# Optimization experiments

Measured on AMD Instinct MI355X. Metric: run time of the kernel, lower is better.

The kernel has to match this reference:

```python
import jax, jax.numpy as jnp
import numpy as np

# dims: batch, history P, horizon Q, hidden D, nodes N, cells C=H*W, Z channels
B_, P_, Q_, D_, N_, C_, H_, W_, CZ = 16, 12, 12, 64, 2000, 1024, 32, 32, 2
K_DIFF = 3  # max diffusion step of DCGRUCell -> K+1 Chebyshev terms


def _mlp2(x, w1, b1, w2, b2):
    return jax.nn.relu(x @ w1 + b1) @ w2 + b2


def _st_embedding(SE, TE, sw1, sb1, sw2, sb2, tw1, tb1, tw2, tb2):
    # GMAN-style spatio-temporal embedding: SE (M,D), TE (B,P,2) ints
    se = _mlp2(SE, sw1, sb1, sw2, sb2)                                  # (M, D)
    te = jnp.concatenate([jax.nn.one_hot(TE[..., 0], 7, dtype=SE.dtype),
                          jax.nn.one_hot(TE[..., 1], 288, dtype=SE.dtype)], axis=-1)
    te = _mlp2(te, tw1, tb1, tw2, tb2)                                  # (B, P, D)
    return se[None, None] + te[:, :, None, :]                           # (B, P, M, D)


def _scaled_laplacian(adj):
    # DCRNN 'laplacian' filter: L_tilde = 2 L / lambda_max - I, lambda_max ~= 2
    A = jnp.maximum(adj, adj.T)
    d = A.sum(axis=1)
    dinv = jnp.where(d > 0, jax.lax.rsqrt(d), 0.0)
    eye = jnp.eye(A.shape[0], dtype=A.dtype)
    L = eye - (dinv[:, None] * A) * dinv[None, :]
    return L - eye


def _gconv(x, L, K):
    # Chebyshev diffusion features: x (B,N,F) -> (B,N,F*(K+1))
    xs = [x, jnp.einsum('nm,bmf->bnf', L, x)]
    for _ in range(2, K + 1):
        xs.append(2.0 * jnp.einsum('nm,bmf->bnf', L, xs[-1]) - xs[-2])
    b, n, f = x.shape
    return jnp.stack(xs, axis=-1).reshape(b, n, f * (K + 1))


def _hard_sigmoid(x):
    return jnp.clip(0.2 * x + 0.5, 0.0, 1.0)


def _conv2d(x, w):
    return jax.lax.conv_general_dilated(x, w, (1, 1), 'SAME',
        dimension_numbers=('NHWC', 'HWIO', 'NHWC'))


def _forward(X, Z, TE, adj_gg, adj_gr, gumbel_noise, se_x, se_z, movement_logits,
             stex_se_w1, stex_se_b1, stex_se_w2, stex_se_b2,
             stex_te_w1, stex_te_b1, stex_te_w2, stex_te_b2,
             stez_se_w1, stez_se_b1, stez_se_w2, stez_se_b2,
             stez_te_w1, stez_te_b1, stez_te_w2, stez_te_b2,
             fcs_z_w1, fcs_z_b1, fcs_z_w2, fcs_z_b2,
             fcs_x_in_w1, fcs_x_in_b1, fcs_x_in_w2, fcs_x_in_b2,
             mov_fc_w, mov_fc_b,
             fcs_x_out_w1, fcs_x_out_b1, fcs_x_out_w2, fcs_x_out_b2,
             convlstm_wx, convlstm_wh,
             dcgru_gate_w, dcgru_gate_b, dcgru_cand_w, dcgru_cand_b):
    B = X.shape[0]
    TEp = TE.astype(jnp.int32)[:, :P_, :]
    # --- cell branch ---
    STEZ = _st_embedding(se_z, TEp, stez_se_w1, stez_se_b1, stez_se_w2, stez_se_b2,
                         stez_te_w1, stez_te_b1, stez_te_w2, stez_te_b2)
    Zf = _mlp2(Z, fcs_z_w1, fcs_z_b1, fcs_z_w2, fcs_z_b2) + STEZ          # (B,P,C,D)
    Zg = Zf.reshape(B, P_, H_, W_, D_)
    def clstm_step(carry, x):
        h, c = carry
        gates = _conv2d(x, convlstm_wx) + _conv2d(h, convlstm_wh)         # (B,H,W,4D)
        i, f, g, o = jnp.split(gates, 4, axis=-1)
        c = _hard_sigmoid(f) * c + _hard_sigmoid(i) * jnp.tanh(g)
        h = _hard_sigmoid(o) * jnp.tanh(c)
        return (h, c), h
    hc0 = (jnp.zeros((B, H_, W_, D_), X.dtype), jnp.zeros((B, H_, W_, D_), X.dtype))
    _, hs = jax.lax.scan(clstm_step, hc0, jnp.swapaxes(Zg, 0, 1))
    Zc = jnp.swapaxes(hs, 0, 1).reshape(B, P_, C_, D_)
    # gumbel-softmax routing over cells (soft, tau=1)
    g = -jnp.log(-jnp.log(gumbel_noise + 1e-20) + 1e-20)
    mZ = jax.nn.softmax(movement_logits + g, axis=-1)                     # (C,C)
    Zc = jnp.einsum('cd,bpdk->bpck', mZ, Zc)
    Zc = jax.nn.relu(Zc @ mov_fc_w + mov_fc_b)
    ZX = jnp.einsum('nc,bpck->bpnk', adj_gr, Zc)                          # (B,P,N,D)
    # --- node branch ---
    STEX = _st_embedding(se_x, TEp, stex_se_w1, stex_se_b1, stex_se_w2, stex_se_b2,
                         stex_te_w1, stex_te_b1, stex_te_w2, stex_te_b2)
    Xf = _mlp2(X[..., None], fcs_x_in_w1, fcs_x_in_b1, fcs_x_in_w2, fcs_x_in_b2) + STEX + ZX
    L = _scaled_laplacian(adj_gg)
    def dcgru_step(h, x):
        xh = jnp.concatenate([x, h], axis=-1)                             # (B,N,2D)
        ru = jax.nn.sigmoid(_gconv(xh, L, K_DIFF) @ dcgru_gate_w + dcgru_gate_b)
        r, u = jnp.split(ru, 2, axis=-1)
        cnd = jnp.tanh(_gconv(jnp.concatenate([x, r * h], axis=-1), L, K_DIFF)
                       @ dcgru_cand_w + dcgru_cand_b)
        return u * h + (1.0 - u) * cnd, None
    h_last, _ = jax.lax.scan(dcgru_step, jnp.zeros((B, N_, D_), X.dtype),
                             jnp.swapaxes(Xf, 0, 1))                      # (B,N,D)
    Y = _mlp2(h_last, fcs_x_out_w1, fcs_x_out_b1, fcs_x_out_w2, fcs_x_out_b2)  # (B,N,Q)
    return jnp.transpose(Y, (0, 2, 1))                                    # (B,Q,N)


def setup_inputs() -> dict:
    key = jax.random.key(0)
    ks = iter(jax.random.split(key, 64))
    def rn(shape, s=0.05):
        return jax.random.normal(next(ks), shape, dtype=jnp.float32) * s
    def ru(shape):
        return jax.random.uniform(next(ks), shape, dtype=jnp.float32)
    z = lambda *s: jnp.zeros(s, jnp.float32)
    NM = K_DIFF + 1
    inp = {
        'X': rn((B_, P_, N_), 1.0),
        'Z': rn((B_, P_, C_, CZ), 1.0),
        'TE': jax.random.randint(next(ks), (B_, P_ + Q_, 2), 0, 7, dtype=jnp.int32),
        'adj_gg': ru((N_, N_)),
        'adj_gr': ru((N_, C_)) * 0.01,
        'gumbel_noise': jnp.clip(ru((C_, C_)), 1e-6, 1.0 - 1e-6),
        'se_x': rn((N_, D_)), 'se_z': rn((C_, D_)),
        'movement_logits': rn((C_, C_)),
        'stex_se_w1': rn((D_, D_)), 'stex_se_b1': z(D_), 'stex_se_w2': rn((D_, D_)), 'stex_se_b2': z(D_),
        'stex_te_w1': rn((295, D_)), 'stex_te_b1': z(D_), 'stex_te_w2': rn((D_, D_)), 'stex_te_b2': z(D_),
        'stez_se_w1': rn((D_, D_)), 'stez_se_b1': z(D_), 'stez_se_w2': rn((D_, D_)), 'stez_se_b2': z(D_),
        'stez_te_w1': rn((295, D_)), 'stez_te_b1': z(D_), 'stez_te_w2': rn((D_, D_)), 'stez_te_b2': z(D_),
        'fcs_z_w1': rn((CZ, D_)), 'fcs_z_b1': z(D_), 'fcs_z_w2': rn((D_, D_)), 'fcs_z_b2': z(D_),
        'fcs_x_in_w1': rn((1, D_)), 'fcs_x_in_b1': z(D_), 'fcs_x_in_w2': rn((D_, D_)), 'fcs_x_in_b2': z(D_),
        'mov_fc_w': rn((D_, D_)), 'mov_fc_b': z(D_),
        'fcs_x_out_w1': rn((D_, D_)), 'fcs_x_out_b1': z(D_), 'fcs_x_out_w2': rn((D_, Q_)), 'fcs_x_out_b2': z(Q_),
        'convlstm_wx': rn((3, 3, D_, 4 * D_)), 'convlstm_wh': rn((3, 3, D_, 4 * D_)),
        'dcgru_gate_w': rn((2 * D_ * NM, 2 * D_)), 'dcgru_gate_b': z(2 * D_),
        'dcgru_cand_w': rn((2 * D_ * NM, D_)), 'dcgru_cand_b': z(D_),
    }
    return inp


def reference(X, Z, TE, adj_gg, adj_gr, gumbel_noise, se_x, se_z, movement_logits,
              stex_se_w1, stex_se_b1, stex_se_w2, stex_se_b2,
              stex_te_w1, stex_te_b1, stex_te_w2, stex_te_b2,
              stez_se_w1, stez_se_b1, stez_se_w2, stez_se_b2,
              stez_te_w1, stez_te_b1, stez_te_w2, stez_te_b2,
              fcs_z_w1, fcs_z_b1, fcs_z_w2, fcs_z_b2,
              fcs_x_in_w1, fcs_x_in_b1, fcs_x_in_w2, fcs_x_in_b2,
              mov_fc_w, mov_fc_b,
              fcs_x_out_w1, fcs_x_out_b1, fcs_x_out_w2, fcs_x_out_b2,
              convlstm_wx, convlstm_wh,
              dcgru_gate_w, dcgru_gate_b, dcgru_cand_w, dcgru_cand_b):
    return _forward(X, Z, TE, adj_gg, adj_gr, gumbel_noise, se_x, se_z, movement_logits,
                    stex_se_w1, stex_se_b1, stex_se_w2, stex_se_b2,
                    stex_te_w1, stex_te_b1, stex_te_w2, stex_te_b2,
                    stez_se_w1, stez_se_b1, stez_se_w2, stez_se_b2,
                    stez_te_w1, stez_te_b1, stez_te_w2, stez_te_b2,
                    fcs_z_w1, fcs_z_b1, fcs_z_w2, fcs_z_b2,
                    fcs_x_in_w1, fcs_x_in_b1, fcs_x_in_w2, fcs_x_in_b2,
                    mov_fc_w, mov_fc_b,
                    fcs_x_out_w1, fcs_x_out_b1, fcs_x_out_w2, fcs_x_out_b2,
                    convlstm_wx, convlstm_wh,
                    dcgru_gate_w, dcgru_gate_b, dcgru_cand_w, dcgru_cand_b)
```

## Files before the change

kernel.cpp:

```cpp
#include <hip/hip_runtime.h>
#include <hip/hip_bf16.h>
#include <math.h>

typedef _Float16 fp16;
typedef _Float16 f16x8 __attribute__((ext_vector_type(8)));
typedef float f32x4 __attribute__((ext_vector_type(4)));

#define BB 16
#define PP 12
#define QQ 12
#define NN 2000
#define CC 1024
#define GP 34
#define GP2 1156

static __device__ __forceinline__ float ldf(float v) { return v; }
static __device__ __forceinline__ float ldf(fp16 v) { return (float)v; }
static __device__ __forceinline__ void stf(float* p, float v) { *p = v; }
static __device__ __forceinline__ void stf(fp16* p, float v) { *p = (fp16)v; }

static __device__ __forceinline__ void gload_lds16(const fp16* g, fp16* l) {
  __builtin_amdgcn_global_load_lds(
      (const __attribute__((address_space(1))) void*)g,
      (__attribute__((address_space(3))) void*)l, 16, 0, 0);
}

__global__ void k_f2h(fp16* __restrict__ dst, const float* __restrict__ src, long long n) {
  long long i = (long long)blockIdx.x * 256 + threadIdx.x;
  if (i < n) dst[i] = (fp16)src[i];
}

__global__ void k_wcatT(fp16* __restrict__ dst, const float* __restrict__ w39,
                        const float* __restrict__ w40) {
  int i = blockIdx.x * 256 + threadIdx.x;
  if (i >= 1152 * 256) return;
  int n = i & 255, kk = i >> 8;
  float v = (kk < 576) ? w39[kk * 256 + n] : w40[(kk - 576) * 256 + n];
  dst[(long long)n * 1152 + kk] = (fp16)v;
}

__global__ void k_gru_repackT(fp16* __restrict__ dst, const float* __restrict__ src, int O) {
  int i = blockIdx.x * 256 + threadIdx.x;
  if (i >= O * 512) return;
  int d = i >> 9;
  int kc = i & 511;
  int t = kc >> 7;
  int c = kc & 127;
  dst[i] = (fp16)src[(c * 4 + t) * O + d];
}

__global__ void k_w2T(fp16* __restrict__ dst, const float* __restrict__ src) {
  int i = blockIdx.x * 256 + threadIdx.x;
  if (i >= 4096) return;
  int d = i >> 6, k = i & 63;
  dst[i] = (fp16)src[k * 64 + d];
}

__global__ void k_dinv(const float* __restrict__ adj, float* __restrict__ dinv) {
  int row = blockIdx.x;
  float s = 0.f;
  for (int j = threadIdx.x; j < NN; j += 256)
    s += fmaxf(adj[(long long)row * NN + j], adj[(long long)j * NN + row]);
  __shared__ float red[256];
  red[threadIdx.x] = s;
  __syncthreads();
  for (int st = 128; st > 0; st >>= 1) {
    if (threadIdx.x < st) red[threadIdx.x] += red[threadIdx.x + st];
    __syncthreads();
  }
  if (threadIdx.x == 0) {
    float d = red[0];
    dinv[row] = d > 0.f ? 1.0f / sqrtf(d) : 0.f;
  }
}

__global__ void k_L(const float* __restrict__ adj, const float* __restrict__ dinv,
                    fp16* __restrict__ Lh) {
  long long i = (long long)blockIdx.x * 256 + threadIdx.x;
  if (i >= (long long)NN * NN) return;
  int r = (int)(i / NN), c = (int)(i % NN);
  float a = fmaxf(adj[(long long)r * NN + c], adj[(long long)c * NN + r]);
  Lh[(long long)r * 2048 + c] = (fp16)(-dinv[r] * a * dinv[c]);
}

__global__ void k_subdiag(fp16* __restrict__ M2) {
  int i = blockIdx.x * 256 + threadIdx.x;
  if (i >= NN) return;
  M2[(long long)i * 2048 + i] = (fp16)((float)M2[(long long)i * 2048 + i] - 1.0f);
}

__global__ void k_gumbel_softmax(const float* __restrict__ ml, const float* __restrict__ gn,
                                 fp16* __restrict__ mZ) {
  int row = blockIdx.x;
  __shared__ float buf[CC];
  __shared__ float red[256];
  int t = threadIdx.x;
  float mx = -1e30f;
  for (int j = t; j < CC; j += 256) {
    float u = gn[(long long)row * CC + j];
    float g = -logf(-logf(u + 1e-20f) + 1e-20f);
    float v = ml[(long long)row * CC + j] + g;
    buf[j] = v;
    mx = fmaxf(mx, v);
  }
  red[t] = mx;
  __syncthreads();
  for (int st = 128; st > 0; st >>= 1) {
    if (t < st) red[t] = fmaxf(red[t], red[t + st]);
// ... 78 lines not shown
  float acc[4][4] = {};
  for (int k0 = 0; k0 < K; k0 += 16) {
#pragma unroll
    for (int j = 0; j < 4; ++j) {
      int e = tid + 256 * j;
      int m = e >> 4, kk = e & 15;
      int gm = row0 + m;
      As[kk][m] = (gm < M) ? ldf(A[(long long)gm * lda + k0 + kk]) : 0.f;
    }
#pragma unroll
    for (int j = 0; j < 4; ++j) {
      int e = tid + 256 * j;
      int kk = e >> 6, n = e & 63;
      int gn = col0 + n;
      Bs[kk][n] = (gn < Ncols) ? ldf(Bm[(long long)(k0 + kk) * ldb + gn]) : 0.f;
    }
    __syncthreads();
#pragma unroll
    for (int kk = 0; kk < 16; ++kk) {
      float a[4], bb[4];
#pragma unroll
      for (int i = 0; i < 4; ++i) a[i] = As[kk][ty * 4 + i];
#pragma unroll
      for (int j = 0; j < 4; ++j) bb[j] = Bs[kk][tx * 4 + j];
#pragma unroll
      for (int i = 0; i < 4; ++i)
#pragma unroll
        for (int j = 0; j < 4; ++j) acc[i][j] = fmaf(a[i], bb[j], acc[i][j]);
    }
    __syncthreads();
  }
#pragma unroll
  for (int i = 0; i < 4; ++i) {
    int r = row0 + ty * 4 + i;
    if (r >= M) continue;
#pragma unroll
    for (int j = 0; j < 4; ++j) {
      int cn = col0 + tx * 4 + j;
      if (cn >= Ncols) continue;
      float v = alpha * acc[i][j];
      if (bias) v += bias[cn];
      if (S) v += beta * ldf(S[(long long)r * ldc + cn]);
      if (act == 1) v = fmaxf(v, 0.f);
      else if (act == 2) v = 1.f / (1.f + expf(-v));
      else if (act == 3) v = tanhf(v);
      stf(&Cm[(long long)r * ldc + cn], v);
    }
  }
}

template <int MT, int MODE>
__global__ __launch_bounds__(256) void mfma7(
    const fp16* __restrict__ A,
    const fp16* __restrict__ U0base, long long uZ, int bHi,
    const fp16* __restrict__ xB, long long xZ,
    const fp16* __restrict__ Xc, long long XcSlab, int Xcld, int Xczmul,
    const fp16* __restrict__ Hc, long long HcSlab, int Hcld, int Hczmul,
    fp16* __restrict__ C, int ldc, long long cBatch,
    const float* __restrict__ bias,
    fp16* __restrict__ rhOut, const fp16* __restrict__ hIn,
    const fp16* __restrict__ uIn, long long uStride,
    int M, int Ncols) {
  __shared__ fp16 As[2][MT * 32];
  __shared__ fp16 Bs[2][64 * 32];
  const int z = blockIdx.z;
  const int n0 = blockIdx.y * 64;
  const fp16* U0z = U0base + (long long)z * uZ;
  const fp16* xBz = xB + (long long)z * xZ;
  C += (long long)z * cBatch;
  if (rhOut) rhOut += (long long)z * uZ;
  if (hIn) hIn += (long long)z * uZ;
  if (uIn) uIn += (long long)z * uStride;
  const int tid = threadIdx.x;
  const int lane = tid & 63, wv = tid >> 6;
  const int wr = wv >> 1, wc = wv & 1;
  const int quad = lane >> 4, ln = lane & 15;
  constexpr int WM = MT / 32;

  const fp16* aSrc[MT / 64];
#pragma unroll
  for (int i = 0; i < MT / 64; ++i) {
    int c = i * 256 + tid;
    int row = c >> 2;
    int lseg = (c & 3) ^ (row & 3);
    aSrc[i] = A + (long long)row * 512 + lseg * 8;
  }
  const int brow = tid >> 2;
  const int blseg = (tid & 3) ^ (brow & 3);
  const long long bnode = n0 + brow;

  f32x4 acc[WM][2];
#pragma unroll
  for (int i = 0; i < WM; ++i)
#pragma unroll
    for (int j = 0; j < 2; ++j) acc[i][j] = (f32x4){0.f, 0.f, 0.f, 0.f};

  auto stage = [&](int t, int buf) {
    const int k0 = t * 32;
#pragma unroll
    for (int i = 0; i < MT / 64; ++i)
      gload_lds16(aSrc[i] + k0, &As[buf][(i * 256 + tid) * 8]);
    if (k0 < 128) {
      int kin = k0 + (tid & 31);
      int ngrp = tid >> 5;
      int n = n0 + ngrp * 8;
      const fp16* src = (kin < 64) ? (xBz + (long long)kin * 2048 + n)
                                   : (U0z + (long long)(kin + bHi) * 2048 + n);
      f16x8 v = *(const f16x8*)src;
      int kk = tid & 31;
#pragma unroll
      for (int j = 0; j < 8; ++j) {
        int rn = ngrp * 8 + j;
        Bs[buf][rn * 32 + ((((kk >> 3) ^ (rn & 3)) << 3) | (kk & 7))] = v[j];
      }
    } else {
      int slab = k0 >> 7;
      int kin = (k0 & 127) + blseg * 8;
      const fp16* src;
      if (kin < 64)
        src = Xc + (long long)(slab - 1) * XcSlab + bnode * Xcld +
              (long long)z * Xczmul + kin;
      else
        src = Hc + (long long)(slab - 1) * HcSlab + bnode * Hcld +
              (long long)z * Hczmul + (kin - 64);
      gload_lds16(src, &Bs[buf][tid * 8]);
    }
  };

  const int sw = (quad ^ (ln & 3)) << 3;
  stage(0, 0);
  for (int t = 0; t < 16; ++t) {
    const int buf = t & 1;
    __syncthreads();
    if (t + 1 < 16) stage(t + 1, buf ^ 1);
    f16x8 af[WM], bf[2];
#pragma unroll
    for (int wm = 0; wm < WM; ++wm) {
      int row = wr * (MT / 2) + wm * 16 + ln;
      af[wm] = *(const f16x8*)&As[buf][row * 32 + sw];
    }
#pragma unroll
    for (int wn = 0; wn < 2; ++wn) {
      int row = wc * 32 + wn * 16 + ln;
      bf[wn] = *(const f16x8*)&Bs[buf][row * 32 + sw];
    }
#pragma unroll
    for (int wm = 0; wm < WM; ++wm)
#pragma unroll
      for (int wn = 0; wn < 2; ++wn)
        acc[wm][wn] =
            __builtin_amdgcn_mfma_f32_16x16x32_f16(af[wm], bf[wn], acc[wm][wn], 0, 0, 0);
  }
#pragma unroll
  for (int wm = 0; wm < WM; ++wm) {
#pragma unroll
    for (int wn = 0; wn < 2; ++wn) {
#pragma unroll
      for (int r = 0; r < 4; ++r) {
        int gm = wr * (MT / 2) + wm * 16 + quad * 4 + r;
        int gn = n0 + wc * 32 + wn * 16 + ln;
        if (gm < M && gn < Ncols) {
          float v = acc[wm][wn][r];
          v += bias[gm];
          if (MODE == 1) {
            v = 1.f / (1.f + expf(-v));
            C[(long long)gm * ldc + gn] = (fp16)v;
            if (gm < 64) {
              float h = (float)hIn[(long long)gm * 2048 + gn];
              rhOut[(long long)gm * 2048 + gn] = (fp16)(v * h);
            }
          } else {
            v = tanhf(v);
            float u = (float)uIn[(long long)(64 + gm) * NN + gn];
            long long ci = (long long)gm * ldc + gn;
            float h = (float)C[ci];
            C[ci] = (fp16)(u * h + (1.f - u) * v);
          }
        }
      }
    }
  }
}

template <int MT, int NT>
__global__ __launch_bounds__(256) void mfma3(
    const fp16* __restrict__ A, int lda, long long zA, int aMsh, long long aMslab,
    const fp16* __restrict__ B, int ldb, long long zB,
    fp16* __restrict__ C, int ldc, long long zC, int cMsh, long long cMslab, int cNsh,
    long long cNslab,
    const fp16* __restrict__ S, long long zS, float beta,
    const float* __restrict__ rowBias, long long zRB,
    const float* __restrict__ s2T, int s2ld,
    int M, int Ncols, int K, float alpha, int act) {
  __shared__ fp16 As[MT][40];
  __shared__ fp16 Bs[NT][40];
  const int z = blockIdx.z;
  const int gm0 = blockIdx.x * MT, n0 = blockIdx.y * NT;
  A += (long long)z * zA;
  B += (long long)z * zB;
  C += (long long)z * zC;
  if (S) S += (long long)z * zS;
  const int tid = threadIdx.x;
  const int lane = tid & 63, wv = tid >> 6;
  const int wr = wv >> 1, wc = wv & 1;
  const int quad = lane >> 4, ln = lane & 15;
  const unsigned aMmask = (1u << aMsh) - 1u;
  const unsigned cMmask = (1u << cMsh) - 1u;
  const unsigned cNmask = (1u << cNsh) - 1u;
  constexpr int WM = MT / 32, WN = NT / 32;
  f32x4 acc[WM][WN];
#pragma unroll
  for (int i = 0; i < WM; ++i)
// ... 23 lines not shown
      int n = c >> 2, seg = c & 3;
      int gn = n0 + n;
      int kk0 = k0 + seg * 8;
      const fp16* src = B + (long long)gn * ldb + kk0;
      if (gn < Ncols && kk0 + 8 <= K) {
        *(f16x8*)&Bs[n][seg * 8] = *(const f16x8*)src;
      } else {
#pragma unroll
        for (int j = 0; j < 8; ++j)
          Bs[n][seg * 8 + j] = (gn < Ncols && kk0 + j < K) ? src[j] : (fp16)0.f;
      }
    }
    __syncthreads();
    f16x8 af[WM], bf[WN];
#pragma unroll
    for (int wm = 0; wm < WM; ++wm)
      af[wm] = *(const f16x8*)&As[wr * (MT / 2) + wm * 16 + ln][quad * 8];
#pragma unroll
    for (int wn = 0; wn < WN; ++wn)
      bf[wn] = *(const f16x8*)&Bs[wc * (NT / 2) + wn * 16 + ln][quad * 8];
#pragma unroll
    for (int wm = 0; wm < WM; ++wm)
#pragma unroll
      for (int wn = 0; wn < WN; ++wn)
        acc[wm][wn] =
            __builtin_amdgcn_mfma_f32_16x16x32_f16(af[wm], bf[wn], acc[wm][wn], 0, 0, 0);
    __syncthreads();
  }
#pragma unroll
  for (int wm = 0; wm < WM; ++wm) {
#pragma unroll
    for (int wn = 0; wn < WN; ++wn) {
#pragma unroll
      for (int r = 0; r < 4; ++r) {
        int gm = gm0 + wr * (MT / 2) + wm * 16 + quad * 4 + r;
        int gn = n0 + wc * (NT / 2) + wn * 16 + ln;
        if (gm < M && gn < Ncols) {
          float v = alpha * acc[wm][wn][r];
          if (rowBias) v += rowBias[(long long)z * zRB + gm];
          if (s2T) v += s2T[(long long)gn * s2ld + gm];
          long long ci = ((long long)((unsigned)gm >> cMsh)) * cMslab +
                         (long long)(gm & cMmask) * ldc +
                         ((long long)((unsigned)gn >> cNsh)) * cNslab + (gn & cNmask);
          if (S) v += beta * (float)S[ci];
          if (act == 1) v = fmaxf(v, 0.f);
          else if (act == 2) v = 1.f / (1.f + expf(-v));
          else if (act == 3) v = tanhf(v);
          C[ci] = (fp16)v;
        }
      }
    }
  }
}

template <int MT, int NT>
__global__ __launch_bounds__(256) void mfma4(
    const fp16* __restrict__ base0, const fp16* __restrict__ base1, int rsh, int ssh,
    long long z0, long long z1, int lda,
    const fp16* __restrict__ B, int ldb, long long zB,
    fp16* __restrict__ C, int ldc, long long zC, int cMsh, long long cMslab, int cNsh,
    long long cNslab,
    const fp16* __restrict__ S, float alpha, float beta, int K) {
  __shared__ fp16 As[2][MT * 32];
  __shared__ fp16 Bs[2][NT * 32];
  const int tid = threadIdx.x;
  const int z = blockIdx.z;
  const int gm0 = blockIdx.x * MT, n0 = blockIdx.y * NT;
  B += (long long)z * zB;
  C += (long long)z * zC;
  if (S) S += (long long)z * zC;
  const unsigned cMmask = (1u << cMsh) - 1u;
  const unsigned cNmask = (1u << cNsh) - 1u;
  const int lane = tid & 63, wv = tid >> 6;
  const int wr = wv >> 1, wc = wv & 1;
  const int quad = lane >> 4, ln = lane & 15;
  constexpr int WM = MT / 32, WN = NT / 32;

  const fp16* aSrc[MT / 64];
  const fp16* bSrc[NT / 64];
#pragma unroll
  for (int i = 0; i < MT / 64; ++i) {
    int c = i * 256 + tid;
    int row = c >> 2;
    int lseg = (c & 3) ^ (row & 3);
    int gm = gm0 + row;
    unsigned b = (unsigned)gm >> rsh;
    unsigned wi = (unsigned)gm & ((1u << rsh) - 1u);
    unsigned sel = wi >> ssh;
    unsigned r = wi & ((1u << ssh) - 1u);
    const fp16* ab = sel ? (base1 + (long long)b * z1) : (base0 + (long long)b * z0);
    aSrc[i] = ab + (long long)r * lda + lseg * 8;
  }
#pragma unroll
  for (int i = 0; i < NT / 64; ++i) {
    int c = i * 256 + tid;
    int row = c >> 2;
    int lseg = (c & 3) ^ (row & 3);
    bSrc[i] = B + (long long)(n0 + row) * ldb + lseg * 8;
  }

  f32x4 acc[WM][WN];
#pragma unroll
  for (int i = 0; i < WM; ++i)
#pragma unroll
    for (int j = 0; j < WN; ++j) acc[i][j] = (f32x4){0.f, 0.f, 0.f, 0.f};

  const int sw = (quad ^ (ln & 3)) << 3;

#pragma unroll
  for (int i = 0; i < MT / 64; ++i) gload_lds16(aSrc[i], &As[0][(i * 256 + tid) * 8]);
#pragma unroll
  for (int i = 0; i < NT / 64; ++i) gload_lds16(bSrc[i], &Bs[0][(i * 256 + tid) * 8]);

  const int nk = K >> 5;
  for (int t = 0; t < nk; ++t) {
    const int buf = t & 1;
    __syncthreads();
    if (t + 1 < nk) {
      const int k1 = (t + 1) * 32;
#pragma unroll
      for (int i = 0; i < MT / 64; ++i)
        gload_lds16(aSrc[i] + k1, &As[buf ^ 1][(i * 256 + tid) * 8]);
#pragma unroll
      for (int i = 0; i < NT / 64; ++i)
        gload_lds16(bSrc[i] + k1, &Bs[buf ^ 1][(i * 256 + tid) * 8]);
    }
    f16x8 af[WM], bf[WN];
#pragma unroll
    for (int wm = 0; wm < WM; ++wm) {
      int row = wr * (MT / 2) + wm * 16 + ln;
      af[wm] = *(const f16x8*)&As[buf][row * 32 + sw];
    }
#pragma unroll
    for (int wn = 0; wn < WN; ++wn) {
      int row = wc * (NT / 2) + wn * 16 + ln;
      bf[wn] = *(const f16x8*)&Bs[buf][row * 32 + sw];
    }
#pragma unroll
    for (int wm = 0; wm < WM; ++wm)
#pragma unroll
      for (int wn = 0; wn < WN; ++wn)
        acc[wm][wn] =
            __builtin_amdgcn_mfma_f32_16x16x32_f16(af[wm], bf[wn], acc[wm][wn], 0, 0, 0);
  }
#pragma unroll
  for (int wm = 0; wm < WM; ++wm)
#pragma unroll
    for (int wn = 0; wn < WN; ++wn)
#pragma unroll
      for (int r = 0; r < 4; ++r) {
        int gm = gm0 + wr * (MT / 2) + wm * 16 + quad * 4 + r;
        int gn = n0 + wc * (NT / 2) + wn * 16 + ln;
        long long ci = ((long long)((unsigned)gm >> cMsh)) * cMslab +
                       (long long)(gm & cMmask) * ldc +
                       ((long long)((unsigned)gn >> cNsh)) * cNslab + (gn & cNmask);
        float v = alpha * acc[wm][wn][r];
        if (S) v += beta * (float)S[ci];
        C[ci] = (fp16)v;
      }
}

template <int MT, int NT>
__global__ __launch_bounds__(256) void mfma6(
    const fp16* __restrict__ A, int lda,
    const fp16* __restrict__ b0, const fp16* __restrict__ b1, int rsh, int ssh,
    long long z0, long long z1, int ldb,
    fp16* __restrict__ C, int ldc, int cMsh, long long cMslab,
    int K) {
  __shared__ fp16 As[2][MT * 32];
  __shared__ fp16 Bs[2][NT * 32];
  const int tid = threadIdx.x;
  const int gm0 = blockIdx.x * MT, n0 = blockIdx.y * NT;
  const unsigned cMmask = (1u << cMsh) - 1u;
  const int lane = tid & 63, wv = tid >> 6;
  const int wr = wv >> 1, wc = wv & 1;
  const int quad = lane >> 4, ln = lane & 15;
  constexpr int WM = MT / 32, WN = NT / 32;

  const fp16* aSrc[MT / 64];
  const fp16* bSrc[NT / 64];
#pragma unroll
  for (int i = 0; i < MT / 64; ++i) {
    int c = i * 256 + tid;
    int row = c >> 2;
    int lseg = (c & 3) ^ (row & 3);
    aSrc[i] = A + (long long)(gm0 + row) * lda + lseg * 8;
  }
#pragma unroll
  for (int i = 0; i < NT / 64; ++i) {
    int c = i * 256 + tid;
    int row = c >> 2;
    int lseg = (c & 3) ^ (row & 3);
    int gn = n0 + row;
    unsigned b = (unsigned)gn >> rsh;
    unsigned wi = (unsigned)gn & ((1u << rsh) - 1u);
    unsigned sel = wi >> ssh;
    unsigned r = wi & ((1u << ssh) - 1u);
    const fp16* bb = sel ? (b1 + (long long)b * z1) : (b0 + (long long)b * z0);
    bSrc[i] = bb + (long long)r * ldb + lseg * 8;
  }

  f32x4 acc[WM][WN];
#pragma unroll
  for (int i = 0; i < WM; ++i)
#pragma unroll
    for (int j = 0; j < WN; ++j) acc[i][j] = (f32x4){0.f, 0.f, 0.f, 0.f};

  const int sw = (quad ^ (ln & 3)) << 3;

#pragma unroll
  for (int i = 0; i < MT / 64; ++i) gload_lds16(aSrc[i], &As[0][(i * 256 + tid) * 8]);
#pragma unroll
  for (int i = 0; i < NT / 64; ++i) gload_lds16(bSrc[i], &Bs[0][(i * 256 + tid) * 8]);

  const int nk = K >> 5;
  for (int t = 0; t < nk; ++t) {
    const int buf = t & 1;
    __syncthreads();
    if (t + 1 < nk) {
      const int k1 = (t + 1) * 32;
#pragma unroll
      for (int i = 0; i < MT / 64; ++i)
        gload_lds16(aSrc[i] + k1, &As[buf ^ 1][(i * 256 + tid) * 8]);
#pragma unroll
      for (int i = 0; i < NT / 64; ++i)
        gload_lds16(bSrc[i] + k1, &Bs[buf ^ 1][(i * 256 + tid) * 8]);
    }
    f16x8 af[WM], bf[WN];
#pragma unroll
    for (int wm = 0; wm < WM; ++wm) {
      int row = wr * (MT / 2) + wm * 16 + ln;
      af[wm] = *(const f16x8*)&As[buf][row * 32 + sw];
    }
#pragma unroll
    for (int wn = 0; wn < WN; ++wn) {
      int row = wc * (NT / 2) + wn * 16 + ln;
      bf[wn] = *(const f16x8*)&Bs[buf][row * 32 + sw];
    }
#pragma unroll
    for (int wm = 0; wm < WM; ++wm)
#pragma unroll
      for (int wn = 0; wn < WN; ++wn)
        acc[wm][wn] =
            __builtin_amdgcn_mfma_f32_16x16x32_f16(af[wm], bf[wn], acc[wm][wn], 0, 0, 0);
  }
#pragma unroll
  for (int wm = 0; wm < WM; ++wm)
#pragma unroll
    for (int wn = 0; wn < WN; ++wn)
#pragma unroll
      for (int r = 0; r < 4; ++r) {
        int gm = gm0 + wr * (MT / 2) + wm * 16 + quad * 4 + r;
        int gn = n0 + wc * (NT / 2) + wn * 16 + ln;
        long long ci = ((long long)((unsigned)gm >> cMsh)) * cMslab +
                       (long long)(gm & cMmask) * ldc + gn;
        C[ci] = (fp16)acc[wm][wn][r];
      }
}

__global__ __launch_bounds__(256) void k_zxtfin(
    const fp16* __restrict__ w2T, const fp16* __restrict__ Tmat,
    fp16* __restrict__ ZXt, const float* __restrict__ teXb, const float* __restrict__ seX) {
  __shared__ fp16 As[64][72];
  __shared__ fp16 Bs[128][72];
  const int z = blockIdx.z;
  const int n0 = blockIdx.y * 128;
  const fp16* Tz = Tmat + (long long)z * 2048 * 64;
  fp16* Cz = ZXt + (long long)z * 64 * 2048;
  const float* tb = teXb + z * 64;
  const int tid = threadIdx.x;
  const int lane = tid & 63, wv = tid >> 6;
  const int wr = wv >> 1, wc = wv & 1;
  const int quad = lane >> 4, ln = lane & 15;
#pragma unroll
  for (int i = 0; i < 2; ++i) {
    int c = tid + 256 * i;
    int row = c >> 3, seg = c & 7;
    *(f16x8*)&As[row][seg * 8] = *(const f16x8*)(w2T + row * 64 + seg * 8);
  }
#pragma unroll
  for (int i = 0; i < 4; ++i) {
    int c = tid + 256 * i;
    int row = c >> 3, seg = c & 7;
    *(f16x8*)&Bs[row][seg * 8] =
        *(const f16x8*)(Tz + (long long)(n0 + row) * 64 + seg * 8);
  }
  __syncthreads();
  f32x4 acc[2][4];
#pragma unroll
  for (int i = 0; i < 2; ++i)
#pragma unroll
    for (int j = 0; j < 4; ++j) acc[i][j] = (f32x4){0.f, 0.f, 0.f, 0.f};
#pragma unroll
  for (int kt = 0; kt < 2; ++kt) {
    f16x8 af[2], bf[4];
#pragma unroll
    for (int wm = 0; wm < 2; ++wm)
      af[wm] = *(const f16x8*)&As[wr * 32 + wm * 16 + ln][kt * 32 + quad * 8];
#pragma unroll
    for (int wn = 0; wn < 4; ++wn)
      bf[wn] = *(const f16x8*)&Bs[wc * 64 + wn * 16 + ln][kt * 32 + quad * 8];
#pragma unroll
    for (int wm = 0; wm < 2; ++wm)
#pragma unroll
      for (int wn = 0; wn < 4; ++wn)
        acc[wm][wn] =
            __builtin_amdgcn_mfma_f32_16x16x32_f16(af[wm], bf[wn], acc[wm][wn], 0, 0, 0);
  }
#pragma unroll
  for (int wm = 0; wm < 2; ++wm)
#pragma unroll
    for (int wn = 0; wn < 4; ++wn)
#pragma unroll
      for (int r = 0; r < 4; ++r) {
        int gm = wr * 32 + wm * 16 + quad * 4 + r;
        int gn = n0 + wc * 64 + wn * 16 + ln;
        long long ci = (long long)gm * 2048 + gn;
        float v = 0.f;
        if (gn < NN)
          v = acc[wm][wn][r] + (float)Cz[ci] + tb[gm] + seX[(long long)gn * 64 + gm];
        Cz[ci] = (fp16)v;
      }
}

__global__ __launch_bounds__(256) void k_conv4(
    const fp16* __restrict__ Zfp, const fp16* __restrict__ hp,
    const fp16* __restrict__ wcatT, fp16* __restrict__ gates, int p) {
  __shared__ fp16 As[2][128 * 32];
  __shared__ fp16 Bs[2][64 * 32];
  const int gm0 = blockIdx.x * 128, n0 = blockIdx.y * 64;
  const int tid = threadIdx.x;
  const int lane = tid & 63, wv = tid >> 6;
  const int wr = wv >> 1, wc = wv & 1;
  const int quad = lane >> 4, ln = lane & 15;

  long long aZ[2], aH[2];
#pragma unroll
  for (int i = 0; i < 2; ++i) {
    int c = tid + 256 * i;
    int row = c >> 2;
    int lseg = (c & 3) ^ (row & 3);
    int m = gm0 + row;
    int b = m >> 10, y = (m >> 5) & 31, x = m & 31;
    int pc = (y + 1) * GP + (x + 1);
    aZ[i] = ((long long)(b * PP + p) * GP2 + pc) * 64 + lseg * 8;
    aH[i] = ((long long)b * GP2 + pc) * 64 + lseg * 8;
  }
  const fp16* bBase;
  {
    int row = tid >> 2;
    int lseg = (tid & 3) ^ (row & 3);
    bBase = wcatT + (long long)(n0 + row) * 1152 + lseg * 8;
  }
  f32x4 acc[4][2];
#pragma unroll
  for (int i = 0; i < 4; ++i)
#pragma unroll
    for (int j = 0; j < 2; ++j) acc[i][j] = (f32x4){0.f, 0.f, 0.f, 0.f};

  auto stage = [&](int t, int buf) {
    int tap = (t >> 1) % 9, half = t & 1;
    int srcsel = t >= 18;
    int off = ((tap / 3 - 1) * GP + (tap % 3 - 1)) * 64 + half * 32;
#pragma unroll
    for (int i = 0; i < 2; ++i) {
      const fp16* src = srcsel ? (hp + aH[i] + off) : (Zfp + aZ[i] + off);
      gload_lds16(src, &As[buf][(i * 256 + tid) * 8]);
    }
    gload_lds16(bBase + t * 32, &Bs[buf][tid * 8]);
  };
  stage(0, 0);
  const int sw = (quad ^ (ln & 3)) << 3;
  for (int t = 0; t < 36; ++t) {
    const int buf = t & 1;
    __syncthreads();
    if (t + 1 < 36) stage(t + 1, buf ^ 1);
    f16x8 af[4], bf[2];
#pragma unroll
    for (int wm = 0; wm < 4; ++wm) {
      int row = wr * 64 + wm * 16 + ln;
      af[wm] = *(const f16x8*)&As[buf][row * 32 + sw];
    }
#pragma unroll
    for (int wn = 0; wn < 2; ++wn) {
      int row = wc * 32 + wn * 16 + ln;
      bf[wn] = *(const f16x8*)&Bs[buf][row * 32 + sw];
    }
#pragma unroll
    for (int wm = 0; wm < 4; ++wm)
#pragma unroll
      for (int wn = 0; wn < 2; ++wn)
        acc[wm][wn] =
            __builtin_amdgcn_mfma_f32_16x16x32_f16(af[wm], bf[wn], acc[wm][wn], 0, 0, 0);
  }
#pragma unroll
  for (int wm = 0; wm < 4; ++wm)
#pragma unroll
    for (int wn = 0; wn < 2; ++wn)
#pragma unroll
      for (int r = 0; r < 4; ++r) {
        int gm = gm0 + wr * 64 + wm * 16 + quad * 4 + r;
        int gn = n0 + wc * 32 + wn * 16 + ln;
        gates[(long long)gm * 256 + gn] = (fp16)acc[wm][wn][r];
      }
}

__global__ void k_clstm_update(const fp16* __restrict__ gates, float* __restrict__ c,
                               fp16* __restrict__ h, fp16* __restrict__ ZclT, int p) {
  long long i = (long long)blockIdx.x * 256 + threadIdx.x;
  if (i >= (long long)BB * CC * 64) return;
  int d = (int)(i & 63);
  long long bc = i >> 6;
  int b = (int)(bc >> 10);
  int cell = (int)(bc & 1023);
  const fp16* g = gates + (((long long)b * CC) + cell) * 256;
  float gi = (float)g[d], gf = (float)g[64 + d], gg = (float)g[128 + d],
        go = (float)g[192 + d];
  float hs_f = fminf(fmaxf(0.2f * gf + 0.5f, 0.f), 1.f);
  float hs_i = fminf(fmaxf(0.2f * gi + 0.5f, 0.f), 1.f);
  float hs_o = fminf(fmaxf(0.2f * go + 0.5f, 0.f), 1.f);
  float cv = hs_f * c[i] + hs_i * tanhf(gg);
  c[i] = cv;
  float hv = hs_o * tanhf(cv);
  int pc = ((cell >> 5) + 1) * GP + (cell & 31) + 1;
  h[((long long)b * GP2 + pc) * 64 + d] = (fp16)hv;
  ZclT[(((long long)(b * PP + p)) * 64 + d) * CC + cell] = (fp16)hv;
}

__global__ void k_tmat(const float* __restrict__ X, const float* __restrict__ w1,
                       const float* __restrict__ b1, fp16* __restrict__ T, long long nrows) {
  long long i = (long long)blockIdx.x * 256 + threadIdx.x;
  if (i >= nrows * 64) return;
  int j = (int)(i & 63);
  long long row = i >> 6;
  int z = (int)(row / NN);
  int n = (int)(row - (long long)z * NN);
  T[(((long long)z * 2048) + n) * 64 + j] = (fp16)fmaxf(X[row] * w1[j] + b1[j], 0.f);
}

__global__ void k_trT(const fp16* __restrict__ U0, float* __restrict__ htmp) {
  long long i = (long long)blockIdx.x * 256 + threadIdx.x;
  if (i >= (long long)BB * NN * 64) return;
  int d = (int)(i & 63);
  long long bn = i >> 6;
  int b = (int)(bn / NN);
  int n = (int)(bn % NN);
  htmp[i] = (float)U0[((long long)b * 192 + 64 + d) * 2048 + n];
}

__global__ void k_out(const float* __restrict__ Y, float* __restrict__ out) {
  int i = blockIdx.x * 256 + threadIdx.x;
  if (i >= BB * QQ * NN) return;
  int n = i % NN;
  int bq = i / NN;
  int b = bq / QQ, q = bq % QQ;
  out[i] = Y[((long long)b * NN + n) * 12 + q];
}

template <typename TA, typename TB, typename TC>
static void launch_gemm(hipStream_t stream, const TA* A, int lda, long long sA,
                        const TB* Bm, int ldb, long long sB, TC* Cm, int ldc, long long sC,
                        const TC* S, long long sS, const float* bias, int M, int Nc, int K,
                        float alpha, float beta, int act, int batch) {
  dim3 g((M + 63) / 64, (Nc + 63) / 64, batch);
  gemm_t<TA, TB, TC><<<g, dim3(256), 0, stream>>>(A, lda, sA, Bm, ldb, sB, Cm, ldc, sC, S,
                                                  sS, bias, M, Nc, K, alpha, beta, act);
}

extern "C" void kernel_launch(void* const* d_in, const int* in_sizes, int n_in,
                              void* d_out, int out_size, void* d_ws, size_t ws_size,
                              hipStream_t stream) {
  char* base = (char*)d_ws;
  size_t off = 0;
  auto alloc_bytes = [&](size_t nb) -> char* {
    char* p = base + off;
    off += (nb + 255) & ~(size_t)255;
    return p;
  };
  auto allocf = [&](size_t n) -> float* { return (float*)alloc_bytes(n * 4); };
  auto alloch = [&](size_t n) -> fp16* { return (fp16*)alloc_bytes(n * 2); };

  const float* X = (const float*)d_in[0];
  const float* Z = (const float*)d_in[1];
  const int* TE = (const int*)d_in[2];
  const float* adj_gg = (const float*)d_in[3];
  const float* adj_gr = (const float*)d_in[4];
  const float* gumbel = (const float*)d_in[5];
  const float* se_x = (const float*)d_in[6];
  const float* se_z = (const float*)d_in[7];
  const float* movement = (const float*)d_in[8];
  auto W = [&](int i) { return (const float*)d_in[i]; };

  fp16* wcatT = alloch((size_t)256 * 1152);
  fp16* gwT = alloch(128 * 512);
  fp16* cwT = alloch(64 * 512);
  fp16* w2T = alloch(64 * 64);
  fp16* w2mT = alloch(64 * 64);
  float* dinv = allocf(NN);
  fp16* LMall = alloch((size_t)6144 * 2048);
  fp16* mZh = alloch((size_t)CC * CC);
  fp16* agh2 = alloch((size_t)2048 * CC);
  float* seZ = allocf(CC * 64);
  float* teZ = allocf(BB * PP * 64);
  float* seX = allocf(NN * 64);
  float* teXb = allocf(BB * PP * 64);
  float* mtmp = allocf(NN * 64);
  float* tetmp = allocf(BB * PP * 64);
  fp16* ruT = alloch((size_t)BB * 128 * NN);
  char* pool = alloc_bytes(50331648);
  fp16* Uall = (fp16*)pool;
  fp16* gates = (fp16*)pool;
  fp16* chh = (fp16*)(pool + 8388608);
  float* ccc = (float*)(pool + 12582912);
  fp16* Zmix = (fp16*)pool;
  fp16* ZmovT = (fp16*)(pool + 25165824);
  fp16* zpool = alloch((size_t)BB * PP * 64 * 2048);
  fp16* Zfp = zpool;
  fp16* ZXt = zpool;
  fp16* Zc = alloch((size_t)BB * PP * CC * 64);

  if (off > ws_size) return;

  const long long TnXSlab = 2048LL * 12288;
  size_t tnxBytes = ((size_t)3 * TnXSlab * 2 + 255) & ~(size_t)255;
  fp16* TnX = (fp16*)(base + off);
  const bool hoist = (off + tnxBytes) <= ws_size;

  const long long uB = 192LL * 2048;
  const long long USL = 16LL * uB;
  const long long ZXB = 12LL * 64 * 2048;
  fp16* Lh = LMall;
  fp16* M2h = LMall + 2048LL * 2048;
  fp16* M3h = LMall + 4096LL * 2048;
  const int KCH = 2016;

  k_wcatT<<<dim3(1152), dim3(256), 0, stream>>>(wcatT, W(39), W(40));
  k_gru_repackT<<<dim3(256), dim3(256), 0, stream>>>(gwT, W(41), 128);
  k_gru_repackT<<<dim3(128), dim3(256), 0, stream>>>(cwT, W(43), 64);
  k_w2T<<<dim3(16), dim3(256), 0, stream>>>(w2T, W(31));
  k_w2T<<<dim3(16), dim3(256), 0, stream>>>(w2mT, W(33));
  k_dinv<<<dim3(NN), dim3(256), 0, stream>>>(adj_gg, dinv);
  hipMemsetAsync(LMall, 0, (size_t)6144 * 2048 * 2, stream);
  k_L<<<dim3((NN * NN + 255) / 256), dim3(256), 0, stream>>>(adj_gg, dinv, Lh);
  mfma4<64, 128><<<dim3(32, 16, 1), dim3(256), 0, stream>>>(
      Lh, Lh, 31, 31, 0LL, 0LL, 2048, Lh, 2048, 0LL, M2h, 2048, 0LL, 31, 0LL, 31, 0LL,
      (const fp16*)nullptr, 2.f, 0.f, KCH);
  k_subdiag<<<dim3((NN + 255) / 256), dim3(256), 0, stream>>>(M2h);
  mfma4<64, 128><<<dim3(32, 16, 1), dim3(256), 0, stream>>>(
      Lh, Lh, 31, 31, 0LL, 0LL, 2048, M2h, 2048, 0LL, M3h, 2048, 0LL, 31, 0LL, 31, 0LL,
      (const fp16*)Lh, 2.f, -1.f, KCH);
  k_gumbel_softmax<<<dim3(CC), dim3(256), 0, stream>>>(movement, gumbel, mZh);
  k_f2h<<<dim3((NN * CC + 255) / 256), dim3(256), 0, stream>>>(agh2, adj_gr,
                                                               (long long)NN * CC);
  hipMemsetAsync(agh2 + (size_t)NN * CC, 0, (size_t)(2048 - NN) * CC * 2, stream);

  launch_gemm(stream, se_z, 64, 0LL, W(17), 64, 0LL, mtmp, 64, 0LL, (float*)nullptr, 0LL,
              W(18), CC, 64, 64, 1.f, 0.f, 1, 1);
  launch_gemm(stream, (const float*)mtmp, 64, 0LL, W(19), 64, 0LL, seZ, 64, 0LL,
              (float*)nullptr, 0LL, W(20), CC, 64, 64, 1.f, 0.f, 0, 1);
  k_te<<<dim3((BB * PP * 64 + 255) / 256), dim3(256), 0, stream>>>(TE, W(21), W(22), tetmp);
  launch_gemm(stream, (const float*)tetmp, 64, 0LL, W(23), 64, 0LL, teZ, 64, 0LL,
              (float*)nullptr, 0LL, W(24), BB * PP, 64, 64, 1.f, 0.f, 0, 1);
  launch_gemm(stream, se_x, 64, 0LL, W(9), 64, 0LL, mtmp, 64, 0LL, (float*)nullptr, 0LL,
              W(10), NN, 64, 64, 1.f, 0.f, 1, 1);
  launch_gemm(stream, (const float*)mtmp, 64, 0LL, W(11), 64, 0LL, seX, 64, 0LL,
              (float*)nullptr, 0LL, W(12), NN, 64, 64, 1.f, 0.f, 0, 1);
  k_te<<<dim3((BB * PP * 64 + 255) / 256), dim3(256), 0, stream>>>(TE, W(13), W(14), tetmp);
  launch_gemm(stream, (const float*)tetmp, 64, 0LL, W(15), 64, 0LL, teXb, 64, 0LL,
              (float*)nullptr, 0LL, W(16), BB * PP, 64, 64, 1.f, 0.f, 0, 1);
  k_addb<<<dim3((BB * PP * 64 + 255) / 256), dim3(256), 0, stream>>>(teXb, W(32),
                                                                     BB * PP * 64);

  long long nZ = (long long)BB * PP * CC * 64;
  k_zf1<<<dim3((int)((nZ + 255) / 256)), dim3(256), 0, stream>>>(Z, W(25), W(26), Zc);
  launch_gemm(stream, (const fp16*)Zc, 64, 0LL, W(27), 64, 0LL, (fp16*)pool, 64, 0LL,
              (fp16*)nullptr, 0LL, W(28), BB * PP * CC, 64, 64, 1.f, 0.f, 0, 1);
  hipMemsetAsync(zpool, 0, (size_t)BB * PP * GP2 * 64 * 2, stream);
  k_add_stez<<<dim3((int)((nZ + 255) / 256)), dim3(256), 0, stream>>>(Zfp, (fp16*)pool,
                                                                      seZ, teZ);

  hipMemsetAsync(chh, 0, (size_t)BB * GP2 * 64 * 2, stream);
  hipMemsetAsync(ccc, 0, (size_t)BB * CC * 64 * 4, stream);
  for (int p = 0; p < PP; ++p) {
    k_conv4<<<dim3(BB * CC / 128, 4), dim3(256), 0, stream>>>(Zfp, chh, wcatT, gates, p);
    k_clstm_update<<<dim3((int)(((long long)BB * CC * 64 + 255) / 256)), dim3(256), 0,
                     stream>>>(gates, ccc, chh, Zc, p);
  }

  mfma4<128, 64><<<dim3(8, 1, 192), dim3(256), 0, stream>>>(
      mZh, mZh, 31, 31, 0LL, 0LL, CC, (const fp16*)Zc, CC, (long long)64 * CC, Zmix, 64,
      (long long)CC * 64, 31, 0LL, 31, 0LL, (const fp16*)nullptr, 1.f, 0.f, CC);
  mfma3<64, 128><<<dim3(1, 8, 192), dim3(256), 0, stream>>>(
      w2mT, 64, 0LL, 31, 0LL, Zmix, 64, (long long)CC * 64, ZmovT, CC, (long long)64 * CC,
      31, 0LL, 31, 0LL, (const fp16*)nullptr, 0LL, 0.f, W(34), 0LL, nullptr, 0, 64, CC, 64,
      1.f, 1);

  mfma4<128, 128><<<dim3(96, 16, 1), dim3(256), 0, stream>>>(
      ZmovT, ZmovT, 31, 31, 0LL, 0LL, 1024, agh2, 1024, 0LL, ZXt, 2048, 0LL, 31, 0LL, 31,
      0LL, (const fp16*)nullptr, 1.f, 0.f, 1024);

  fp16* Tmat = Zc;
  for (int half = 0; half < 2; ++half) {
    long long z0 = 96LL * half;
    k_tmat<<<dim3((int)((96LL * NN * 64 + 255) / 256)), dim3(256), 0, stream>>>(
        X + z0 * NN, W(29), W(30), Tmat, 96LL * NN);
    k_zxtfin<<<dim3(1, 16, 96), dim3(256), 0, stream>>>(
        w2T, Tmat, ZXt + z0 * 64 * 2048, teXb + z0 * 64, seX);
  }

  fp16* U0 = Uall;
  fp16* Tn = Uall + USL;
  fp16* Tn2 = Uall + 3 * USL;
  const long long TnSlab = 2048LL * 2048;
  const long long TnHSlab = 2048LL * 1024;
  const long long Tn2Slab = 2048LL * 1024;
  hipMemsetAsync(U0, 0, (size_t)USL * 2, stream);

  if (hoist) {
    mfma6<128, 128><<<dim3(48, 96), dim3(256), 0, stream>>>(
        LMall, 2048, ZXt, ZXt, 31, 31, 0LL, 0LL, 2048, TnX, 12288, 11, TnXSlab, KCH);
  }

  for (int p = 0; p < PP; ++p) {
    const fp16* xP = ZXt + (long long)p * 64 * 2048;
    if (hoist) {
      mfma6<128, 128><<<dim3(48, 8), dim3(256), 0, stream>>>(
          LMall, 2048, U0 + 64 * 2048, U0 + 64 * 2048, 6, 6, uB, uB, 2048, Tn, 1024, 11,
          TnHSlab, KCH);
      mfma7<128, 1><<<dim3(1, 32, BB), dim3(256), 0, stream>>>(
          gwT, U0, uB, 0, xP, ZXB,
          TnX + (long long)p * 64, TnXSlab, 12288, 768,
          Tn, TnHSlab, 1024, 64,
          ruT, NN, (long long)128 * NN, W(42), U0 + 128 * 2048, U0 + 64 * 2048,
          (const fp16*)nullptr, 0LL, 128, NN);
    } else {
      mfma6<128, 128><<<dim3(48, 16), dim3(256), 0, stream>>>(
          LMall, 2048, xP, U0 + 64 * 2048, 7, 6, ZXB, uB, 2048, Tn, 2048, 11, TnSlab, KCH);
      mfma7<128, 1><<<dim3(1, 32, BB), dim3(256), 0, stream>>>(
          gwT, U0, uB, 0, xP, ZXB,
          Tn, TnSlab, 2048, 128,
          Tn + 64, TnSlab, 2048, 128,
          ruT, NN, (long long)128 * NN, W(42), U0 + 128 * 2048, U0 + 64 * 2048,
          (const fp16*)nullptr, 0LL, 128, NN);
    }
    mfma6<128, 128><<<dim3(48, 8), dim3(256), 0, stream>>>(
        LMall, 2048, U0 + 128 * 2048, U0 + 128 * 2048, 6, 6, uB, uB, 2048, Tn2, 1024, 11,
        Tn2Slab, KCH);
    if (hoist) {
      mfma7<64, 2><<<dim3(1, 32, BB), dim3(256), 0, stream>>>(
          cwT, U0, uB, 64, xP, ZXB,
          TnX + (long long)p * 64, TnXSlab, 12288, 768,
          Tn2, Tn2Slab, 1024, 64,
          U0 + 64 * 2048, 2048, uB, W(44), (fp16*)nullptr, (const fp16*)nullptr,
          (const fp16*)ruT, (long long)128 * NN, 64, NN);
    } else {
      mfma7<64, 2><<<dim3(1, 32, BB), dim3(256), 0, stream>>>(
          cwT, U0, uB, 64, xP, ZXB,
          Tn, TnSlab, 2048, 128,
          Tn2, Tn2Slab, 1024, 64,
          U0 + 64 * 2048, 2048, uB, W(44), (fp16*)nullptr, (const fp16*)nullptr,
          (const fp16*)ruT, (long long)128 * NN, 64, NN);
    }
  }

  float* htmp = (float*)Zc;
  float* out1 = (float*)(Zc + 5120000);
  float* out2 = (float*)(Zc + 10240000);
  k_trT<<<dim3((int)(((long long)BB * NN * 64 + 255) / 256)), dim3(256), 0, stream>>>(U0,
                                                                                      htmp);
  launch_gemm(stream, (const float*)htmp, 64, 0LL, W(35), 64, 0LL, out1, 64, 0LL,
              (float*)nullptr, 0LL, W(36), BB * NN, 64, 64, 1.f, 0.f, 1, 1);
  launch_gemm(stream, (const float*)out1, 64, 0LL, W(37), 12, 0LL, out2, 12, 0LL,
              (float*)nullptr, 0LL, W(38), BB * NN, 12, 64, 1.f, 0.f, 0, 1);
  k_out<<<dim3((BB * QQ * NN + 255) / 256), dim3(256), 0, stream>>>(out2, (float*)d_out);
}
```

Baseline: 2.998 ms.

## Change LDS XOR swizzle to row-pair key and drop hoisted X diffusion path

Every MFMA GEMM kernel now keys its LDS XOR swizzle on (row>>1)&3 instead of row&3. This changes which 16-byte segment each row lands in, to reduce LDS bank conflicts on the f16x8 fragment reads. The hoisted precomputation of Chebyshev diffusion terms for all input timesteps (TnX) is also removed. The loop always recomputes the X and hidden-state diffusion together per step, trading a large workspace buffer and an up-front GEMM for wider per-step GEMMs.

```diff
diff --git a/kernel.cpp b/kernel.cpp
--- a/kernel.cpp
+++ b/kernel.cpp
@@ -24,6 +24,7 @@
       (const __attribute__((address_space(1))) void*)g,
       (__attribute__((address_space(3))) void*)l, 16, 0, 0);
 }
+
 
 __global__ void k_f2h(fp16* __restrict__ dst, const float* __restrict__ src, long long n) {
   long long i = (long long)blockIdx.x * 256 + threadIdx.x;
@@ -268,11 +269,11 @@
   for (int i = 0; i < MT / 64; ++i) {
     int c = i * 256 + tid;
     int row = c >> 2;
-    int lseg = (c & 3) ^ (row & 3);
+    int lseg = (c & 3) ^ ((c >> 3) & 3);
     aSrc[i] = A + (long long)row * 512 + lseg * 8;
   }
   const int brow = tid >> 2;
-  const int blseg = (tid & 3) ^ (brow & 3);
+  const int blseg = (tid & 3) ^ ((tid >> 3) & 3);
   const long long bnode = n0 + brow;
 
   f32x4 acc[WM][2];
@@ -297,7 +298,7 @@
 #pragma unroll
       for (int j = 0; j < 8; ++j) {
         int rn = ngrp * 8 + j;
-        Bs[buf][rn * 32 + ((((kk >> 3) ^ (rn & 3)) << 3) | (kk & 7))] = v[j];
+        Bs[buf][rn * 32 + ((((kk >> 3) ^ ((rn >> 1) & 3)) << 3) | (kk & 7))] = v[j];
       }
     } else {
       int slab = k0 >> 7;
@@ -313,7 +314,7 @@
     }
   };
 
-  const int sw = (quad ^ (ln & 3)) << 3;
+  const int sw = (quad ^ ((ln >> 1) & 3)) << 3;
   stage(0, 0);
   for (int t = 0; t < 16; ++t) {
     const int buf = t & 1;
@@ -503,7 +504,7 @@
   for (int i = 0; i < MT / 64; ++i) {
     int c = i * 256 + tid;
     int row = c >> 2;
-    int lseg = (c & 3) ^ (row & 3);
+    int lseg = (c & 3) ^ ((c >> 3) & 3);
     int gm = gm0 + row;
     unsigned b = (unsigned)gm >> rsh;
     unsigned wi = (unsigned)gm & ((1u << rsh) - 1u);
@@ -515,9 +516,8 @@
 #pragma unroll
   for (int i = 0; i < NT / 64; ++i) {
     int c = i * 256 + tid;
-    int row = c >> 2;
-    int lseg = (c & 3) ^ (row & 3);
-    bSrc[i] = B + (long long)(n0 + row) * ldb + lseg * 8;
+    int lseg = (c & 3) ^ ((c >> 3) & 3);
+    bSrc[i] = B + (long long)(n0 + (c >> 2)) * ldb + lseg * 8;
   }
 
   f32x4 acc[WM][WN];
@@ -526,7 +526,7 @@
 #pragma unroll
     for (int j = 0; j < WN; ++j) acc[i][j] = (f32x4){0.f, 0.f, 0.f, 0.f};
 
-  const int sw = (quad ^ (ln & 3)) << 3;
+  const int sw = (quad ^ ((ln >> 1) & 3)) << 3;
 
 #pragma unroll
   for (int i = 0; i < MT / 64; ++i) gload_lds16(aSrc[i], &As[0][(i * 256 + tid) * 8]);
@@ -603,16 +603,14 @@
 #pragma unroll
   for (int i = 0; i < MT / 64; ++i) {
     int c = i * 256 + tid;
-    int row = c >> 2;
-    int lseg = (c & 3) ^ (row & 3);
-    aSrc[i] = A + (long long)(gm0 + row) * lda + lseg * 8;
+    int lseg = (c & 3) ^ ((c >> 3) & 3);
+    aSrc[i] = A + (long long)(gm0 + (c >> 2)) * lda + lseg * 8;
   }
 #pragma unroll
   for (int i = 0; i < NT / 64; ++i) {
     int c = i * 256 + tid;
-    int row = c >> 2;
-    int lseg = (c & 3) ^ (row & 3);
-    int gn = n0 + row;
+    int lseg = (c & 3) ^ ((c >> 3) & 3);
+    int gn = n0 + (c >> 2);
     unsigned b = (unsigned)gn >> rsh;
     unsigned wi = (unsigned)gn & ((1u << rsh) - 1u);
     unsigned sel = wi >> ssh;
@@ -627,7 +625,7 @@
 #pragma unroll
     for (int j = 0; j < WN; ++j) acc[i][j] = (f32x4){0.f, 0.f, 0.f, 0.f};
 
-  const int sw = (quad ^ (ln & 3)) << 3;
+  const int sw = (quad ^ ((ln >> 1) & 3)) << 3;
 
 #pragma unroll
   for (int i = 0; i < MT / 64; ++i) gload_lds16(aSrc[i], &As[0][(i * 256 + tid) * 8]);
@@ -760,7 +758,7 @@
   for (int i = 0; i < 2; ++i) {
     int c = tid + 256 * i;
     int row = c >> 2;
-    int lseg = (c & 3) ^ (row & 3);
+    int lseg = (c & 3) ^ ((c >> 3) & 3);
     int m = gm0 + row;
     int b = m >> 10, y = (m >> 5) & 31, x = m & 31;
     int pc = (y + 1) * GP + (x + 1);
@@ -770,7 +768,7 @@
   const fp16* bBase;
   {
     int row = tid >> 2;
-    int lseg = (tid & 3) ^ (row & 3);
+    int lseg = (tid & 3) ^ ((tid >> 3) & 3);
     bBase = wcatT + (long long)(n0 + row) * 1152 + lseg * 8;
   }
   f32x4 acc[4][2];
@@ -791,7 +789,7 @@
     gload_lds16(bBase + t * 32, &Bs[buf][tid * 8]);
   };
   stage(0, 0);
-  const int sw = (quad ^ (ln & 3)) << 3;
+  const int sw = (quad ^ ((ln >> 1) & 3)) << 3;
   for (int t = 0; t < 36; ++t) {
     const int buf = t & 1;
     __syncthreads();
@@ -942,11 +940,6 @@
 
   if (off > ws_size) return;
 
-  const long long TnXSlab = 2048LL * 12288;
-  size_t tnxBytes = ((size_t)3 * TnXSlab * 2 + 255) & ~(size_t)255;
-  fp16* TnX = (fp16*)(base + off);
-  const bool hoist = (off + tnxBytes) <= ws_size;
-
   const long long uB = 192LL * 2048;
   const long long USL = 16LL * uB;
   const long long ZXB = 12LL * 64 * 2048;
@@ -1033,55 +1026,28 @@
   fp16* Tn = Uall + USL;
   fp16* Tn2 = Uall + 3 * USL;
   const long long TnSlab = 2048LL * 2048;
-  const long long TnHSlab = 2048LL * 1024;
   const long long Tn2Slab = 2048LL * 1024;
   hipMemsetAsync(U0, 0, (size_t)USL * 2, stream);
 
-  if (hoist) {
-    mfma6<128, 128><<<dim3(48, 96), dim3(256), 0, stream>>>(
-        LMall, 2048, ZXt, ZXt, 31, 31, 0LL, 0LL, 2048, TnX, 12288, 11, TnXSlab, KCH);
-  }
-
   for (int p = 0; p < PP; ++p) {
     const fp16* xP = ZXt + (long long)p * 64 * 2048;
-    if (hoist) {
-      mfma6<128, 128><<<dim3(48, 8), dim3(256), 0, stream>>>(
-          LMall, 2048, U0 + 64 * 2048, U0 + 64 * 2048, 6, 6, uB, uB, 2048, Tn, 1024, 11,
-          TnHSlab, KCH);
-      mfma7<128, 1><<<dim3(1, 32, BB), dim3(256), 0, stream>>>(
-          gwT, U0, uB, 0, xP, ZXB,
-          TnX + (long long)p * 64, TnXSlab, 12288, 768,
-          Tn, TnHSlab, 1024, 64,
-          ruT, NN, (long long)128 * NN, W(42), U0 + 128 * 2048, U0 + 64 * 2048,
-          (const fp16*)nullptr, 0LL, 128, NN);
-    } else {
-      mfma6<128, 128><<<dim3(48, 16), dim3(256), 0, stream>>>(
-          LMall, 2048, xP, U0 + 64 * 2048, 7, 6, ZXB, uB, 2048, Tn, 2048, 11, TnSlab, KCH);
-      mfma7<128, 1><<<dim3(1, 32, BB), dim3(256), 0, stream>>>(
-          gwT, U0, uB, 0, xP, ZXB,
-          Tn, TnSlab, 2048, 128,
-          Tn + 64, TnSlab, 2048, 128,
-          ruT, NN, (long long)128 * NN, W(42), U0 + 128 * 2048, U0 + 64 * 2048,
-          (const fp16*)nullptr, 0LL, 128, NN);
-    }
+    mfma6<128, 128><<<dim3(48, 16), dim3(256), 0, stream>>>(
+        LMall, 2048, xP, U0 + 64 * 2048, 7, 6, ZXB, uB, 2048, Tn, 2048, 11, TnSlab, KCH);
+    mfma7<128, 1><<<dim3(1, 32, BB), dim3(256), 0, stream>>>(
+        gwT, U0, uB, 0, xP, ZXB,
+        Tn, TnSlab, 2048, 128,
+        Tn + 64, TnSlab, 2048, 128,
+        ruT, NN, (long long)128 * NN, W(42), U0 + 128 * 2048, U0 + 64 * 2048,
+        (const fp16*)nullptr, 0LL, 128, NN);
     mfma6<128, 128><<<dim3(48, 8), dim3(256), 0, stream>>>(
         LMall, 2048, U0 + 128 * 2048, U0 + 128 * 2048, 6, 6, uB, uB, 2048, Tn2, 1024, 11,
         Tn2Slab, KCH);
-    if (hoist) {
-      mfma7<64, 2><<<dim3(1, 32, BB), dim3(256), 0, stream>>>(
-          cwT, U0, uB, 64, xP, ZXB,
-          TnX + (long long)p * 64, TnXSlab, 12288, 768,
-          Tn2, Tn2Slab, 1024, 64,
-          U0 + 64 * 2048, 2048, uB, W(44), (fp16*)nullptr, (const fp16*)nullptr,
-          (const fp16*)ruT, (long long)128 * NN, 64, NN);
-    } else {
-      mfma7<64, 2><<<dim3(1, 32, BB), dim3(256), 0, stream>>>(
-          cwT, U0, uB, 64, xP, ZXB,
-          Tn, TnSlab, 2048, 128,
-          Tn2, Tn2Slab, 1024, 64,
-          U0 + 64 * 2048, 2048, uB, W(44), (fp16*)nullptr, (const fp16*)nullptr,
-          (const fp16*)ruT, (long long)128 * NN, 64, NN);
-    }
+    mfma7<64, 2><<<dim3(1, 32, BB), dim3(256), 0, stream>>>(
+        cwT, U0, uB, 64, xP, ZXB,
+        Tn, TnSlab, 2048, 128,
+        Tn2, Tn2Slab, 1024, 64,
+        U0 + 64 * 2048, 2048, uB, W(44), (fp16*)nullptr, (const fp16*)nullptr,
+        (const fp16*)ruT, (long long)128 * NN, 64, NN);
   }
 
   float* htmp = (float*)Zc;
```

Measured after the change: 2.938 ms. 1.02x faster.
